# Performance work log

Measured on AMD Instinct MI355X. Metric: run time of the kernel, lower is better.

The kernel has to match this reference:

```python
import jax, jax.numpy as jnp
import numpy as np

VOCAB = 50000   # vocab.count
EMBED = 256     # args.embed
B = 16          # batch
C = 64          # uniform context_len per example (stack() requires it)
S = 512         # src_seq == qry_seq == args.max_in_seq
UNK = 1         # vocab.w2i['<UNK>']


def setup_inputs() -> dict:
    key = jax.random.key(0)
    k1, k2, k3, k4 = jax.random.split(key, 4)
    sources = jax.random.randint(k1, (B * C, S), 0, VOCAB)
    # queries: contiguous nonzero prefix of length q_len in [S//2, S], zeros after
    ids = jax.random.randint(k2, (B, S), 1, VOCAB)
    qlens = jax.random.randint(k3, (B,), S // 2, S + 1)
    queries = jnp.where(jnp.arange(S)[None, :] < qlens[:, None], ids, 0)
    emb = jax.random.normal(k4, (VOCAB, EMBED), dtype=jnp.float32)
    return {"sources": sources, "queries": queries, "context_len": C, "emb": emb}


def reference(sources, queries, context_len, emb):
    vocab = emb.shape[0]
    # unk_tensor: clamp out-of-vocab ids to <UNK>
    src_ids = jnp.where(sources >= vocab, UNK, sources)
    q_ids = jnp.where(queries >= vocab, UNK, queries)
    b, s = queries.shape
    # [b, C, S, D] embedded sources; [b, S, D] embedded queries
    es = emb[src_ids].reshape(b, context_len, s, emb.shape[1])
    eq = emb[q_ids]
    # q_len slicing == masking since nonzero query prefix is contiguous
    qmask = (queries > 0).astype(emb.dtype)            # [b, S]
    # score[b,c] = sum_{j < q_len_b} <es[b,c,j], eq[b,j]>
    scores = jnp.einsum('bcsd,bsd->bc', es, eq * qmask[:, :, None])
    sims = jax.nn.softmax(scores, axis=1)              # per-example softmax over context
    top = jnp.argmax(scores, axis=1)                   # argmax of sim == argmax of scores
    src3 = sources.reshape(b, context_len, s)
    out_sources = jnp.take_along_axis(src3, top[:, None, None], axis=1).squeeze(1)
    return out_sources, sims
```

## Files before the change

### kernel.cpp

```cpp
#include <hip/hip_runtime.h>

#define VOCAB 50000
#define EMBED 256
#define NB    16
#define NC    64
#define NS    512
#define UNK   1

#define CTILE 16
#define JT    16
#define JLEN  (NS / JT)
#define BF_TABLE_BYTES ((size_t)VOCAB * EMBED * 2)
#define PARTIAL_ELEMS  (JT * NB * NC)

__device__ __forceinline__ unsigned short f2bf_rne(float f) {
    unsigned int u = __float_as_uint(f);
    u = (u + 0x7fffu + ((u >> 16) & 1u)) >> 16;
    return (unsigned short)u;
}

__global__ __launch_bounds__(256) void convert_kernel(
    const float* __restrict__ emb, unsigned int* __restrict__ bf)
{
    const size_t t = (size_t)blockIdx.x * 256 + threadIdx.x;
    const float4* __restrict__ e4 = (const float4*)emb;
    const float4 a = e4[t * 2];
    const float4 b = e4[t * 2 + 1];
    uint4 r;
    r.x = (unsigned int)f2bf_rne(a.x) | ((unsigned int)f2bf_rne(a.y) << 16);
    r.y = (unsigned int)f2bf_rne(a.z) | ((unsigned int)f2bf_rne(a.w) << 16);
    r.z = (unsigned int)f2bf_rne(b.x) | ((unsigned int)f2bf_rne(b.y) << 16);
    r.w = (unsigned int)f2bf_rne(b.z) | ((unsigned int)f2bf_rne(b.w) << 16);
    ((uint4*)bf)[t] = r;
}

__global__ __launch_bounds__(256) void scores_bf_kernel(
    const int* __restrict__ src, const int* __restrict__ q,
    const float* __restrict__ emb, const unsigned int* __restrict__ bf,
    float* __restrict__ partial)
{
    const int x  = blockIdx.x;
    const int jt = x & (JT - 1);
    const int ct = (x >> 4) & (NC / CTILE - 1);
    const int b  = x >> 6;
    const int c0 = ct * CTILE;
    const int j0 = jt * JLEN;

    const int tid  = threadIdx.x;
    const int wave = tid >> 6;
    const int lane = tid & 63;

    const float4* __restrict__ emb4 = (const float4*)emb;
    const uint2*  __restrict__ bfe  = (const uint2*)bf;
    const int* __restrict__ qrow = q + (size_t)b * NS;
    const int* __restrict__ srow = src + ((size_t)b * NC + c0) * NS;

    __shared__ float qt[JLEN][EMBED];
    __shared__ int   sids[CTILE][JLEN];
    __shared__ int   qids[JLEN];
    __shared__ int   nnz_sh;

    if (tid < 64) {
        const int qv = (tid < JLEN) ? qrow[j0 + tid] : 0;
        if (tid < JLEN) qids[tid] = (qv >= VOCAB) ? UNK : qv;
        const unsigned long long bal = __ballot(qv > 0);
        if (tid == 0) nnz_sh = __popcll(bal);
    }
#pragma unroll
    for (int k = 0; k < 2; k++) {
        const int idx = tid + k * 256;
        const int i   = idx >> 5;
        const int j   = idx & 31;
        const int sv  = srow[(size_t)i * NS + j0 + j];
        sids[i][j] = (sv >= VOCAB) ? UNK : sv;
    }
    __syncthreads();

    const int nnz = nnz_sh;

    float4* qt4 = (float4*)qt;
    for (int r = wave; r < nnz; r += 4)
        qt4[r * 64 + lane] = emb4[(size_t)qids[r] * (EMBED / 4) + lane];
    __syncthreads();

    float acc[CTILE];
#pragma unroll
    for (int i = 0; i < CTILE; i++) acc[i] = 0.f;

    for (int j = wave; j < nnz; j += 4) {
        const float4 qv = qt4[j * 64 + lane];
        uint2 a[CTILE];
#pragma unroll
        for (int i = 0; i < CTILE; i++)
            a[i] = bfe[(size_t)sids[i][j] * 64 + lane];
#pragma unroll
        for (int i = 0; i < CTILE; i++) {
            const float f0 = __uint_as_float(a[i].x << 16);
            const float f1 = __uint_as_float(a[i].x & 0xffff0000u);
            const float f2 = __uint_as_float(a[i].y << 16);
            const float f3 = __uint_as_float(a[i].y & 0xffff0000u);
            acc[i] += f0 * qv.x + f1 * qv.y + f2 * qv.z + f3 * qv.w;
        }
    }

#pragma unroll
    for (int off = 32; off > 0; off >>= 1)
#pragma unroll
        for (int i = 0; i < CTILE; i++)
            acc[i] += __shfl_down(acc[i], off, 64);

    __shared__ float red[4][CTILE];
    if (lane == 0)
#pragma unroll
        for (int i = 0; i < CTILE; i++) red[wave][i] = acc[i];
    __syncthreads();

    if (tid < CTILE) {
        const float s = red[0][tid] + red[1][tid] + red[2][tid] + red[3][tid];
        partial[(size_t)jt * (NB * NC) + b * NC + c0 + tid] = s;
    }
}

__global__ __launch_bounds__(256) void scores_f32_kernel(
    const int* __restrict__ src, const int* __restrict__ q,
    const float* __restrict__ emb, float* __restrict__ partial)
{
    const int x  = blockIdx.x;
    const int jt = x & 7;
    const int ct = (x >> 3) & 7;
    const int b  = x >> 6;
    const int c0 = ct * 8;
    const int j0 = jt * 64;

    const int tid = threadIdx.x, wave = tid >> 6, lane = tid & 63;
    const float4* __restrict__ emb4 = (const float4*)emb;
    const int* __restrict__ qrow = q + (size_t)b * NS;
    const int* __restrict__ srow = src + ((size_t)b * NC + c0) * NS;

    float acc[8];
#pragma unroll
    for (int i = 0; i < 8; i++) acc[i] = 0.f;

    for (int j = j0 + wave; j < j0 + 64; j += 4) {
        const int qv = qrow[j];
        if (qv > 0) {
            const int qid = (qv >= VOCAB) ? UNK : qv;
            const float4 eq = emb4[(size_t)qid * (EMBED / 4) + lane];
            float4 a[8];
#pragma unroll
            for (int i = 0; i < 8; i++) {
                const int sv = srow[(size_t)i * NS + j];
                a[i] = emb4[(size_t)((sv >= VOCAB) ? UNK : sv) * (EMBED / 4) + lane];
            }
#pragma unroll
            for (int i = 0; i < 8; i++)
                acc[i] += a[i].x * eq.x + a[i].y * eq.y + a[i].z * eq.z + a[i].w * eq.w;
        }
    }
#pragma unroll
    for (int off = 32; off > 0; off >>= 1)
#pragma unroll
        for (int i = 0; i < 8; i++)
            acc[i] += __shfl_down(acc[i], off, 64);

    __shared__ float red[4][8];
    if (lane == 0)
#pragma unroll
        for (int i = 0; i < 8; i++) red[wave][i] = acc[i];
    __syncthreads();
    if (tid < 8)
        partial[(size_t)jt * (NB * NC) + b * NC + c0 + tid] =
            red[0][tid] + red[1][tid] + red[2][tid] + red[3][tid];
}

__global__ __launch_bounds__(256) void finalize_kernel(
    const float* __restrict__ partial, const int* __restrict__ src,
    float* __restrict__ out, int jtn)
{
    const int b = blockIdx.x, tid = threadIdx.x;
    __shared__ int top_sh;

    if (tid < 64) {
        float s = 0.f;
        for (int t = 0; t < jtn; t++)
            s += partial[(size_t)t * (NB * NC) + b * NC + tid];

        float m = s;
#pragma unroll
        for (int off = 32; off > 0; off >>= 1)
            m = fmaxf(m, __shfl_xor(m, off, 64));
        const float e = expf(s - m);
        float sum = e;
#pragma unroll
        for (int off = 32; off > 0; off >>= 1)
            sum += __shfl_xor(sum, off, 64);

        out[NB * NS + b * NC + tid] = e / sum;

        const unsigned long long ballot = __ballot(s == m);
        if (tid == 0) top_sh = __ffsll(ballot) - 1;
    }
    __syncthreads();

    const int top = top_sh;
    const int* __restrict__ srow = src + ((size_t)b * NC + top) * NS;
    for (int j = tid; j < NS; j += 256)
        out[b * NS + j] = (float)srow[j];
}

extern "C" void kernel_launch(void* const* d_in, const int* in_sizes, int n_in,
                              void* d_out, int out_size, void* d_ws, size_t ws_size,
                              hipStream_t stream) {
    const int*   src = (const int*)d_in[0];
    const int*   q   = (const int*)d_in[1];
    const float* emb = (const float*)d_in[3];
    float* out = (float*)d_out;

    if (ws_size >= BF_TABLE_BYTES + PARTIAL_ELEMS * sizeof(float)) {
        unsigned int* bf = (unsigned int*)d_ws;
        float* partial = (float*)((char*)d_ws + BF_TABLE_BYTES);
        convert_kernel<<<VOCAB * EMBED / 2048, 256, 0, stream>>>(emb, bf);
        scores_bf_kernel<<<NB * (NC / CTILE) * JT, 256, 0, stream>>>(src, q, emb, bf, partial);
        finalize_kernel<<<NB, 256, 0, stream>>>(partial, src, out, JT);
    } else {
        float* partial = (float*)d_ws;
        scores_f32_kernel<<<NB * 8 * 8, 256, 0, stream>>>(src, q, emb, partial);
        finalize_kernel<<<NB, 256, 0, stream>>>(partial, src, out, 8);
    }
}
```

Before: 131.2 us.

## Split waves into half-wave row groups with 16-byte bf16 gathers and drop query LDS staging

Each wave now splits into two 32-lane halves, each handling 8 context rows. Every lane gathers a 16-byte uint4 of bf16 embedding, so each source row takes 32 lanes instead of 64. Query embeddings are read straight from global memory per step instead of being staged in LDS, and JT doubles to 32 to launch more, smaller blocks with an occupancy hint of 8. The aim is wider memory transactions, fewer registers and no LDS staging barrier, at the cost of repeated query loads and more partial sums for finalize to add up.

After: 158.5 us. 20.9% more time.

```diff
diff --git a/kernel.cpp b/kernel.cpp
--- a/kernel.cpp
+++ b/kernel.cpp
@@ -8,7 +8,7 @@
 #define UNK   1
 
 #define CTILE 16
-#define JT    16
+#define JT    32
 #define JLEN  (NS / JT)
 #define BF_TABLE_BYTES ((size_t)VOCAB * EMBED * 2)
 #define PARTIAL_ELEMS  (JT * NB * NC)
@@ -34,31 +34,32 @@
     ((uint4*)bf)[t] = r;
 }
 
-__global__ __launch_bounds__(256) void scores_bf_kernel(
+__global__ __launch_bounds__(256, 8) void scores_bf_kernel(
     const int* __restrict__ src, const int* __restrict__ q,
     const float* __restrict__ emb, const unsigned int* __restrict__ bf,
     float* __restrict__ partial)
 {
     const int x  = blockIdx.x;
     const int jt = x & (JT - 1);
-    const int ct = (x >> 4) & (NC / CTILE - 1);
-    const int b  = x >> 6;
+    const int ct = (x >> 5) & (NC / CTILE - 1);
+    const int b  = x >> 7;
     const int c0 = ct * CTILE;
     const int j0 = jt * JLEN;
 
     const int tid  = threadIdx.x;
     const int wave = tid >> 6;
     const int lane = tid & 63;
+    const int half = lane >> 5;
+    const int hl   = lane & 31;
 
     const float4* __restrict__ emb4 = (const float4*)emb;
-    const uint2*  __restrict__ bfe  = (const uint2*)bf;
+    const uint4*  __restrict__ bft  = (const uint4*)bf;
     const int* __restrict__ qrow = q + (size_t)b * NS;
     const int* __restrict__ srow = src + ((size_t)b * NC + c0) * NS;
 
-    __shared__ float qt[JLEN][EMBED];
-    __shared__ int   sids[CTILE][JLEN];
-    __shared__ int   qids[JLEN];
-    __shared__ int   nnz_sh;
+    __shared__ int sids[CTILE][JLEN];
+    __shared__ int qids[JLEN];
+    __shared__ int nnz_sh;
 
     if (tid < 64) {
         const int qv = (tid < JLEN) ? qrow[j0 + tid] : 0;
@@ -66,53 +67,58 @@
         const unsigned long long bal = __ballot(qv > 0);
         if (tid == 0) nnz_sh = __popcll(bal);
     }
-#pragma unroll
-    for (int k = 0; k < 2; k++) {
-        const int idx = tid + k * 256;
-        const int i   = idx >> 5;
-        const int j   = idx & 31;
-        const int sv  = srow[(size_t)i * NS + j0 + j];
+    {
+        const int i = tid >> 4;
+        const int j = tid & (JLEN - 1);
+        const int sv = srow[(size_t)i * NS + j0 + j];
         sids[i][j] = (sv >= VOCAB) ? UNK : sv;
     }
     __syncthreads();
 
     const int nnz = nnz_sh;
 
-    float4* qt4 = (float4*)qt;
-    for (int r = wave; r < nnz; r += 4)
-        qt4[r * 64 + lane] = emb4[(size_t)qids[r] * (EMBED / 4) + lane];
-    __syncthreads();
-
-    float acc[CTILE];
-#pragma unroll
-    for (int i = 0; i < CTILE; i++) acc[i] = 0.f;
+    float acc[8];
+#pragma unroll
+    for (int i = 0; i < 8; i++) acc[i] = 0.f;
 
     for (int j = wave; j < nnz; j += 4) {
-        const float4 qv = qt4[j * 64 + lane];
-        uint2 a[CTILE];
-#pragma unroll
-        for (int i = 0; i < CTILE; i++)
-            a[i] = bfe[(size_t)sids[i][j] * 64 + lane];
-#pragma unroll
-        for (int i = 0; i < CTILE; i++) {
-            const float f0 = __uint_as_float(a[i].x << 16);
-            const float f1 = __uint_as_float(a[i].x & 0xffff0000u);
-            const float f2 = __uint_as_float(a[i].y << 16);
-            const float f3 = __uint_as_float(a[i].y & 0xffff0000u);
-            acc[i] += f0 * qv.x + f1 * qv.y + f2 * qv.z + f3 * qv.w;
+        const int qid = qids[j];
+        const float4 q0 = emb4[(size_t)qid * (EMBED / 4) + hl * 2];
+        const float4 q1 = emb4[(size_t)qid * (EMBED / 4) + hl * 2 + 1];
+#pragma unroll
+        for (int mm = 0; mm < 2; mm++) {
+            uint4 g[4];
+#pragma unroll
+            for (int k = 0; k < 4; k++) {
+                const int cc = mm * 4 + k + 8 * half;
+                g[k] = bft[(size_t)sids[cc][j] * 32 + hl];
+            }
+#pragma unroll
+            for (int k = 0; k < 4; k++) {
+                const float f0 = __uint_as_float(g[k].x << 16);
+                const float f1 = __uint_as_float(g[k].x & 0xffff0000u);
+                const float f2 = __uint_as_float(g[k].y << 16);
+                const float f3 = __uint_as_float(g[k].y & 0xffff0000u);
+                const float f4 = __uint_as_float(g[k].z << 16);
+                const float f5 = __uint_as_float(g[k].z & 0xffff0000u);
+                const float f6 = __uint_as_float(g[k].w << 16);
+                const float f7 = __uint_as_float(g[k].w & 0xffff0000u);
+                acc[mm * 4 + k] += f0 * q0.x + f1 * q0.y + f2 * q0.z + f3 * q0.w
+                                 + f4 * q1.x + f5 * q1.y + f6 * q1.z + f7 * q1.w;
+            }
         }
     }
 
 #pragma unroll
-    for (int off = 32; off > 0; off >>= 1)
-#pragma unroll
-        for (int i = 0; i < CTILE; i++)
-            acc[i] += __shfl_down(acc[i], off, 64);
+    for (int off = 16; off > 0; off >>= 1)
+#pragma unroll
+        for (int i = 0; i < 8; i++)
+            acc[i] += __shfl_down(acc[i], off, 32);
 
     __shared__ float red[4][CTILE];
-    if (lane == 0)
-#pragma unroll
-        for (int i = 0; i < CTILE; i++) red[wave][i] = acc[i];
+    if (hl == 0)
+#pragma unroll
+        for (int i = 0; i < 8; i++) red[wave][i + 8 * half] = acc[i];
     __syncthreads();
 
     if (tid < CTILE) {
```

## Partition source-id gathers by vocab range into per-block worklists

Applied to the files above, without the earlier changes.

Replaces the context-tiled scores kernel with one where each block handles a 64-position query slice for all contexts and only the source ids that fall in one eighth of the vocabulary. Each block builds a shared-memory worklist of (id, context, position) entries and gathers the bf16 rows with half-wave 16-byte loads. Query rows are now also read from the bf16 table. The aim is to improve L2 locality of the embedding gathers by spreading vocab ranges across blocks, at the cost of shared atomics, a capped worklist, more partial slices for finalize to sum, and lower query precision.

After: 149.3 us. +13.8%, slower.

```diff
diff --git a/kernel.cpp b/kernel.cpp
--- a/kernel.cpp
+++ b/kernel.cpp
@@ -7,11 +7,14 @@
 #define NS    512
 #define UNK   1
 
-#define CTILE 16
-#define JT    16
-#define JLEN  (NS / JT)
+#define NPART 8
+#define PDIV  ((VOCAB + NPART - 1) / NPART)
+#define PJT   8
+#define PJLEN 64
+#define WLCAP 1024
+#define NSLICE (NPART * PJT)
 #define BF_TABLE_BYTES ((size_t)VOCAB * EMBED * 2)
-#define PARTIAL_ELEMS  (JT * NB * NC)
+#define PARTIAL_ELEMS  (NSLICE * NB * NC)
 
 __device__ __forceinline__ unsigned short f2bf_rne(float f) {
     unsigned int u = __float_as_uint(f);
@@ -34,91 +37,102 @@
     ((uint4*)bf)[t] = r;
 }
 
-__global__ __launch_bounds__(256) void scores_bf_kernel(
+__device__ __forceinline__ float dot_u(unsigned a, unsigned b) {
+    const float a0 = __uint_as_float(a << 16);
+    const float a1 = __uint_as_float(a & 0xffff0000u);
+    const float b0 = __uint_as_float(b << 16);
+    const float b1 = __uint_as_float(b & 0xffff0000u);
+    return a0 * b0 + a1 * b1;
+}
+
+__global__ __launch_bounds__(256) void scores_part_kernel(
     const int* __restrict__ src, const int* __restrict__ q,
-    const float* __restrict__ emb, const unsigned int* __restrict__ bf,
-    float* __restrict__ partial)
-{
-    const int x  = blockIdx.x;
-    const int jt = x & (JT - 1);
-    const int ct = (x >> 4) & (NC / CTILE - 1);
-    const int b  = x >> 6;
-    const int c0 = ct * CTILE;
-    const int j0 = jt * JLEN;
+    const unsigned int* __restrict__ bf, float* __restrict__ partial)
+{
+    const int bid = blockIdx.x;
+    const int p   = bid & (NPART - 1);
+    const int jt  = (bid >> 3) & (PJT - 1);
+    const int b   = bid >> 6;
+    const int j0  = jt * PJLEN;
 
     const int tid  = threadIdx.x;
     const int wave = tid >> 6;
     const int lane = tid & 63;
-
-    const float4* __restrict__ emb4 = (const float4*)emb;
-    const uint2*  __restrict__ bfe  = (const uint2*)bf;
-    const int* __restrict__ qrow = q + (size_t)b * NS;
-    const int* __restrict__ srow = src + ((size_t)b * NC + c0) * NS;
-
-    __shared__ float qt[JLEN][EMBED];
-    __shared__ int   sids[CTILE][JLEN];
-    __shared__ int   qids[JLEN];
-    __shared__ int   nnz_sh;
-
-    if (tid < 64) {
-        const int qv = (tid < JLEN) ? qrow[j0 + tid] : 0;
-        if (tid < JLEN) qids[tid] = (qv >= VOCAB) ? UNK : qv;
-        const unsigned long long bal = __ballot(qv > 0);
-        if (tid == 0) nnz_sh = __popcll(bal);
-    }
-#pragma unroll
-    for (int k = 0; k < 2; k++) {
-        const int idx = tid + k * 256;
-        const int i   = idx >> 5;
-        const int j   = idx & 31;
-        const int sv  = srow[(size_t)i * NS + j0 + j];
-        sids[i][j] = (sv >= VOCAB) ? UNK : sv;
-    }
-    __syncthreads();
-
-    const int nnz = nnz_sh;
-
-    float4* qt4 = (float4*)qt;
-    for (int r = wave; r < nnz; r += 4)
-        qt4[r * 64 + lane] = emb4[(size_t)qids[r] * (EMBED / 4) + lane];
-    __syncthreads();
-
-    float acc[CTILE];
-#pragma unroll
-    for (int i = 0; i < CTILE; i++) acc[i] = 0.f;
-
-    for (int j = wave; j < nnz; j += 4) {
-        const float4 qv = qt4[j * 64 + lane];
-        uint2 a[CTILE];
-#pragma unroll
-        for (int i = 0; i < CTILE; i++)
-            a[i] = bfe[(size_t)sids[i][j] * 64 + lane];
-#pragma unroll
-        for (int i = 0; i < CTILE; i++) {
-            const float f0 = __uint_as_float(a[i].x << 16);
-            const float f1 = __uint_as_float(a[i].x & 0xffff0000u);
-            const float f2 = __uint_as_float(a[i].y << 16);
-            const float f3 = __uint_as_float(a[i].y & 0xffff0000u);
-            acc[i] += f0 * qv.x + f1 * qv.y + f2 * qv.z + f3 * qv.w;
-        }
-    }
-
-#pragma unroll
-    for (int off = 32; off > 0; off >>= 1)
-#pragma unroll
-        for (int i = 0; i < CTILE; i++)
-            acc[i] += __shfl_down(acc[i], off, 64);
-
-    __shared__ float red[4][CTILE];
-    if (lane == 0)
-#pragma unroll
-        for (int i = 0; i < CTILE; i++) red[wave][i] = acc[i];
-    __syncthreads();
-
-    if (tid < CTILE) {
-        const float s = red[0][tid] + red[1][tid] + red[2][tid] + red[3][tid];
-        partial[(size_t)jt * (NB * NC) + b * NC + c0 + tid] = s;
-    }
+    const int half = lane >> 5;
+    const int hl   = lane & 31;
+
+    const uint2* __restrict__ bfe  = (const uint2*)bf;
+    const uint4* __restrict__ bft4 = (const uint4*)bf;
+
+    __shared__ uint2 qt[PJLEN][64];
+    __shared__ unsigned int wl[WLCAP];
+    __shared__ float score_sh[NC];
+    __shared__ int qid_sh[PJLEN];
+    __shared__ int cnt;
+
+    if (tid < PJLEN) {
+        const int qv = q[(size_t)b * NS + j0 + tid];
+        qid_sh[tid] = (qv == 0) ? -1 : ((qv >= VOCAB) ? UNK : qv);
+    }
+    if (tid < NC) score_sh[tid] = 0.f;
+    if (tid == 0) cnt = 0;
+    __syncthreads();
+
+    for (int r = wave; r < PJLEN; r += 4) {
+        const int qid = qid_sh[r];
+        if (qid >= 0)
+            qt[r][lane] = bfe[(size_t)qid * 64 + lane];
+    }
+
+    const int* __restrict__ srow = src + (size_t)b * NC * NS;
+#pragma unroll
+    for (int k = 0; k < 16; k++) {
+        const int idx = k * 256 + tid;
+        const int c   = idx >> 6;
+        const int jj  = idx & 63;
+        int sv = srow[(size_t)c * NS + j0 + jj];
+        sv = (sv >= VOCAB) ? UNK : sv;
+        if (qid_sh[jj] >= 0 && (sv / PDIV) == p) {
+            const int pos = atomicAdd(&cnt, 1);
+            if (pos < WLCAP)
+                wl[pos] = ((unsigned)sv << 12) | (unsigned)(c << 6) | (unsigned)jj;
+        }
+    }
+    __syncthreads();
+
+    const int nE = (cnt < WLCAP) ? cnt : WLCAP;
+
+    for (int e = wave * 2; e < nE; e += 16) {
+        const int eA = e + half;
+        const int eB = e + 8 + half;
+        const bool vA = eA < nE;
+        const bool vB = eB < nE;
+        const unsigned wA = wl[vA ? eA : 0];
+        const unsigned wB = wl[vB ? eB : 0];
+        const int sidA = wA >> 12, cA = (wA >> 6) & 63, jA = wA & 63;
+        const int sidB = wB >> 12, cB = (wB >> 6) & 63, jB = wB & 63;
+        const uint4 gA = bft4[(size_t)sidA * 32 + hl];
+        const uint4 gB = bft4[(size_t)sidB * 32 + hl];
+        const uint4 qA = ((const uint4*)qt[jA])[hl];
+        const uint4 qB = ((const uint4*)qt[jB])[hl];
+        float dA = dot_u(gA.x, qA.x) + dot_u(gA.y, qA.y)
+                 + dot_u(gA.z, qA.z) + dot_u(gA.w, qA.w);
+        float dB = dot_u(gB.x, qB.x) + dot_u(gB.y, qB.y)
+                 + dot_u(gB.z, qB.z) + dot_u(gB.w, qB.w);
+#pragma unroll
+        for (int off = 16; off > 0; off >>= 1) {
+            dA += __shfl_down(dA, off, 32);
+            dB += __shfl_down(dB, off, 32);
+        }
+        if (hl == 0) {
+            if (vA) atomicAdd(&score_sh[cA], dA);
+            if (vB) atomicAdd(&score_sh[cB], dB);
+        }
+    }
+    __syncthreads();
+
+    if (tid < NC)
+        partial[(size_t)(p * PJT + jt) * (NB * NC) + b * NC + tid] = score_sh[tid];
 }
 
 __global__ __launch_bounds__(256) void scores_f32_kernel(
@@ -220,8 +234,8 @@
         unsigned int* bf = (unsigned int*)d_ws;
         float* partial = (float*)((char*)d_ws + BF_TABLE_BYTES);
         convert_kernel<<<VOCAB * EMBED / 2048, 256, 0, stream>>>(emb, bf);
-        scores_bf_kernel<<<NB * (NC / CTILE) * JT, 256, 0, stream>>>(src, q, emb, bf, partial);
-        finalize_kernel<<<NB, 256, 0, stream>>>(partial, src, out, JT);
+        scores_part_kernel<<<NB * PJT * NPART, 256, 0, stream>>>(src, q, bf, partial);
+        finalize_kernel<<<NB, 256, 0, stream>>>(partial, src, out, NSLICE);
     } else {
         float* partial = (float*)d_ws;
         scores_f32_kernel<<<NB * 8 * 8, 256, 0, stream>>>(src, q, emb, partial);
```

## Halve context tile, load bf16 query rows into registers, drop LDS staging

Applied to the files above, without the earlier changes.

Shrinks the context tile from 16 to 8, doubling the block count to 2048. Query embeddings now come from the bf16 table straight into registers, replacing the fp32 rows that were staged in 32 KB of shared memory, which removes a barrier and most of the LDS use. The per-wave j loop is fully unrolled to 8 iterations. This should raise occupancy and parallelism, but it rounds the queries to bf16 as well, adding precision error, and halves reuse of each query row across contexts.

Result: faster. 128.5 us (-2.0%).

```diff
diff --git a/kernel.cpp b/kernel.cpp
--- a/kernel.cpp
+++ b/kernel.cpp
@@ -7,7 +7,7 @@
 #define NS    512
 #define UNK   1
 
-#define CTILE 16
+#define CTILE 8
 #define JT    16
 #define JLEN  (NS / JT)
 #define BF_TABLE_BYTES ((size_t)VOCAB * EMBED * 2)
@@ -36,13 +36,12 @@
 
 __global__ __launch_bounds__(256) void scores_bf_kernel(
     const int* __restrict__ src, const int* __restrict__ q,
-    const float* __restrict__ emb, const unsigned int* __restrict__ bf,
-    float* __restrict__ partial)
+    const unsigned int* __restrict__ bf, float* __restrict__ partial)
 {
     const int x  = blockIdx.x;
     const int jt = x & (JT - 1);
     const int ct = (x >> 4) & (NC / CTILE - 1);
-    const int b  = x >> 6;
+    const int b  = x >> 7;
     const int c0 = ct * CTILE;
     const int j0 = jt * JLEN;
 
@@ -50,15 +49,13 @@
     const int wave = tid >> 6;
     const int lane = tid & 63;
 
-    const float4* __restrict__ emb4 = (const float4*)emb;
-    const uint2*  __restrict__ bfe  = (const uint2*)bf;
+    const uint2* __restrict__ bfe = (const uint2*)bf;
     const int* __restrict__ qrow = q + (size_t)b * NS;
     const int* __restrict__ srow = src + ((size_t)b * NC + c0) * NS;
 
-    __shared__ float qt[JLEN][EMBED];
-    __shared__ int   sids[CTILE][JLEN];
-    __shared__ int   qids[JLEN];
-    __shared__ int   nnz_sh;
+    __shared__ int sids[CTILE][JLEN];
+    __shared__ int qids[JLEN];
+    __shared__ int nnz_sh;
 
     if (tid < 64) {
         const int qv = (tid < JLEN) ? qrow[j0 + tid] : 0;
@@ -66,40 +63,47 @@
         const unsigned long long bal = __ballot(qv > 0);
         if (tid == 0) nnz_sh = __popcll(bal);
     }
-#pragma unroll
-    for (int k = 0; k < 2; k++) {
-        const int idx = tid + k * 256;
-        const int i   = idx >> 5;
-        const int j   = idx & 31;
-        const int sv  = srow[(size_t)i * NS + j0 + j];
+    {
+        const int i  = tid >> 5;
+        const int j  = tid & (JLEN - 1);
+        const int sv = srow[(size_t)i * NS + j0 + j];
         sids[i][j] = (sv >= VOCAB) ? UNK : sv;
     }
     __syncthreads();
 
     const int nnz = nnz_sh;
 
-    float4* qt4 = (float4*)qt;
-    for (int r = wave; r < nnz; r += 4)
-        qt4[r * 64 + lane] = emb4[(size_t)qids[r] * (EMBED / 4) + lane];
-    __syncthreads();
+    uint2 qr[8];
+#pragma unroll
+    for (int it = 0; it < 8; ++it) {
+        const int j = wave + it * 4;
+        qr[it] = (j < nnz) ? bfe[(size_t)qids[j] * 64 + lane]
+                           : make_uint2(0u, 0u);
+    }
 
     float acc[CTILE];
 #pragma unroll
     for (int i = 0; i < CTILE; i++) acc[i] = 0.f;
 
-    for (int j = wave; j < nnz; j += 4) {
-        const float4 qv = qt4[j * 64 + lane];
-        uint2 a[CTILE];
+#pragma unroll
+    for (int it = 0; it < 8; ++it) {
+        const int j = wave + it * 4;
+        if (j >= nnz) break;
+        const float q0 = __uint_as_float(qr[it].x << 16);
+        const float q1 = __uint_as_float(qr[it].x & 0xffff0000u);
+        const float q2 = __uint_as_float(qr[it].y << 16);
+        const float q3 = __uint_as_float(qr[it].y & 0xffff0000u);
+        uint2 g[CTILE];
 #pragma unroll
         for (int i = 0; i < CTILE; i++)
-            a[i] = bfe[(size_t)sids[i][j] * 64 + lane];
+            g[i] = bfe[(size_t)sids[i][j] * 64 + lane];
 #pragma unroll
         for (int i = 0; i < CTILE; i++) {
-            const float f0 = __uint_as_float(a[i].x << 16);
-            const float f1 = __uint_as_float(a[i].x & 0xffff0000u);
-            const float f2 = __uint_as_float(a[i].y << 16);
-            const float f3 = __uint_as_float(a[i].y & 0xffff0000u);
-            acc[i] += f0 * qv.x + f1 * qv.y + f2 * qv.z + f3 * qv.w;
+            const float f0 = __uint_as_float(g[i].x << 16);
+            const float f1 = __uint_as_float(g[i].x & 0xffff0000u);
+            const float f2 = __uint_as_float(g[i].y << 16);
+            const float f3 = __uint_as_float(g[i].y & 0xffff0000u);
+            acc[i] += f0 * q0 + f1 * q1 + f2 * q2 + f3 * q3;
         }
     }
 
@@ -220,7 +224,7 @@
         unsigned int* bf = (unsigned int*)d_ws;
         float* partial = (float*)((char*)d_ws + BF_TABLE_BYTES);
         convert_kernel<<<VOCAB * EMBED / 2048, 256, 0, stream>>>(emb, bf);
-        scores_bf_kernel<<<NB * (NC / CTILE) * JT, 256, 0, stream>>>(src, q, emb, bf, partial);
+        scores_bf_kernel<<<NB * (NC / CTILE) * JT, 256, 0, stream>>>(src, q, bf, partial);
         finalize_kernel<<<NB, 256, 0, stream>>>(partial, src, out, JT);
     } else {
         float* partial = (float*)d_ws;
```
